# Optimization experiments

Measured on AMD Instinct MI355X. Metric: run time of the kernel, lower is better.

## Reference

```python
import jax, jax.numpy as jnp
import numpy as np

NEG_INF = -jnp.inf


def setup_inputs() -> dict:
    key = jax.random.key(0)
    ks = jax.random.split(key, 8)
    B, Lq, Lk, D, H = 8, 2048, 2048, 256, 128
    queries = jax.random.normal(ks[0], (B, Lq, D), dtype=jnp.float32)
    keys = jax.random.normal(ks[1], (B, Lk, D), dtype=jnp.float32)
    values_1 = jax.random.normal(ks[2], (B, Lk, D), dtype=jnp.float32)
    values_2 = jax.random.normal(ks[3], (B, Lq, D), dtype=jnp.float32)
    values_1_mask = jax.random.randint(ks[4], (B, Lk), 0, 2).astype(bool)
    values_2_mask = jax.random.randint(ks[5], (B, Lq), 0, 2).astype(bool)
    # xavier_normal for Linear(D -> H): std = sqrt(2/(D+H))
    std = float(np.sqrt(2.0 / (D + H)))
    Wq = jax.random.normal(ks[6], (H, D), dtype=jnp.float32) * std
    Wk = jax.random.normal(ks[7], (H, D), dtype=jnp.float32) * std
    scaling = jnp.ones((1, H), dtype=jnp.float32)
    return {
        "queries": queries, "keys": keys,
        "values_1": values_1, "values_1_mask": values_1_mask,
        "values_2": values_2, "values_2_mask": values_2_mask,
        "Wq": Wq, "Wk": Wk, "scaling": scaling,
    }


def reference(queries, keys, values_1, values_1_mask, values_2, values_2_mask, Wq, Wk, scaling):
    # projections + relu (eval mode: dropout inactive)
    pq = jax.nn.relu(jnp.einsum("bqd,hd->bqh", queries, Wq))        # [B,Lq,H]
    pk = jax.nn.relu(jnp.einsum("bkd,hd->bkh", keys, Wk)) * scaling  # [B,Lk,H]
    scores = jnp.einsum("bqh,bkh->bqk", pq, pk)                      # [B,Lq,Lk]

    # branch 2: softmax over queries axis of scores^T, masked by values_2_mask [B,Lq]
    scores_T = jnp.where(values_2_mask[:, None, :], NEG_INF, jnp.swapaxes(scores, 1, 2))  # [B,Lk,Lq]
    alpha_2 = jax.nn.softmax(scores_T, axis=2)
    output_2 = jnp.einsum("bkq,bqd->bkd", alpha_2, values_2)         # [B,Lk,D]

    # branch 1: softmax over keys axis, masked by values_1_mask [B,Lk]
    scores_1 = jnp.where(values_1_mask[:, None, :], NEG_INF, scores)  # [B,Lq,Lk]
    alpha_1 = jax.nn.softmax(scores_1, axis=2)
    output = jnp.einsum("bqk,bkd->bqd", alpha_1, values_1)           # [B,Lq,D]

    return (output, output_2)
```

## Files before the change

kernel.cpp:

```cpp
#include <hip/hip_runtime.h>
#include <cstdint>
#include <math.h>

#define B 8
#define L 2048
#define D 256
#define H 128

typedef __attribute__((ext_vector_type(8))) _Float16 half8;
typedef __attribute__((ext_vector_type(4))) _Float16 half4t;
typedef __attribute__((ext_vector_type(2))) _Float16 half2v;
typedef __attribute__((ext_vector_type(4))) float f32x4;
typedef unsigned short ushort;
typedef unsigned int uint;


__global__ void prep_kernel(const void* __restrict__ raw0,
                            const void* __restrict__ raw1,
                            const float* __restrict__ Wq,
                            const float* __restrict__ Wk,
                            float* __restrict__ fb1,
                            float* __restrict__ fb2,
                            _Float16* __restrict__ Wf) {
    const int t = threadIdx.x;
    const int z = blockIdx.y;
    {
        const void* raw = z ? raw1 : raw0;
        float* outb = z ? fb2 : fb1;
        const uint* wd = (const uint*)raw;
        __shared__ int flag;
        if (t == 0) flag = 0;
        __syncthreads();
        if (wd[t] > 1u) flag = 1;
        __syncthreads();
        const int base = blockIdx.x * 1024;
        if (flag) {
            const uint8_t* by = (const uint8_t*)raw;
#pragma unroll
            for (int j = 0; j < 4; ++j) {
                int i = base + t + 256 * j;
                outb[i] = by[i] ? -INFINITY : 0.f;
            }
        } else {
#pragma unroll
            for (int j = 0; j < 4; ++j) {
                int i = base + t + 256 * j;
                outb[i] = wd[i] ? -INFINITY : 0.f;
            }
        }
    }
    {
        const float* Wsrc = z ? Wk : Wq;
        const int chunk = blockIdx.x * 256 + t;
        const int h = chunk >> 5;
        const int d0 = (chunk & 31) * 8;
        float4 v0 = *(const float4*)(Wsrc + (size_t)h * 256 + d0);
        float4 v1 = *(const float4*)(Wsrc + (size_t)h * 256 + d0 + 4);
        half8 hv;
        hv[0] = (_Float16)v0.x; hv[1] = (_Float16)v0.y;
        hv[2] = (_Float16)v0.z; hv[3] = (_Float16)v0.w;
        hv[4] = (_Float16)v1.x; hv[5] = (_Float16)v1.y;
        hv[6] = (_Float16)v1.z; hv[7] = (_Float16)v1.w;
        const int db = d0 >> 5, dq = (d0 >> 3) & 3;
        size_t off = (size_t)z * 32768 +
                     ((size_t)((h >> 4) * 8 + db)) * 512 + dq * 128 + (h & 15) * 8;
        *(half8*)(Wf + off) = hv;
    }
}

__launch_bounds__(256, 2)
__global__ void proj_mfma_kernel(const float* __restrict__ queries,
                                 const float* __restrict__ keys,
                                 const _Float16* __restrict__ Wf,
                                 const float* __restrict__ scaling,
                                 _Float16* __restrict__ pqo,
                                 _Float16* __restrict__ pko) {
    const int t = threadIdx.x;
    const int w = t >> 6;
    const int lane = t & 63;
    const int l15 = lane & 15;
    const int quad = lane >> 4;
    const int z = blockIdx.z;
    const int half = blockIdx.y;
    const int r0 = blockIdx.x * 64;
    const float* in = z ? keys : queries;
    _Float16* outp = z ? pko : pqo;

    __shared__ __attribute__((aligned(16))) _Float16 Wl[32 * 512];
    __shared__ __attribute__((aligned(16))) _Float16 Af[4][8 * 512];

    {
        const _Float16* wsrc = Wf + ((size_t)z * 64 + half * 32) * 512;
#pragma unroll
        for (int i = 0; i < 8; ++i) {
            const int f = w * 8 + i;
            __builtin_amdgcn_global_load_lds(
                (const __attribute__((address_space(1))) uint*)(wsrc + f * 512 + lane * 8),
                (__attribute__((address_space(3))) uint*)(Wl + f * 512 + lane * 8),
                16, 0, 0);
        }
    }
    {
#pragma unroll
        for (int j = 0; j < 16; ++j) {
            const int idx = t + 256 * j;
            const int row = idx >> 6;
            const int c4 = idx & 63;
            float4 v = *(const float4*)(in + ((size_t)(r0 + row)) * 256 + c4 * 4);
            half4t h4;
            h4[0] = (_Float16)v.x; h4[1] = (_Float16)v.y;
            h4[2] = (_Float16)v.z; h4[3] = (_Float16)v.w;
            const int rt = row >> 4, rl = row & 15;
            const int d0 = c4 * 4;
            const int db = d0 >> 5, dq = (d0 >> 3) & 3, e = d0 & 7;
            *(half4t*)(&Af[rt][db * 512 + dq * 128 + rl * 8 + e]) = h4;
        }
    }
    __syncthreads();

    half8 a[8];
#pragma unroll
    for (int db = 0; db < 8; ++db)
        a[db] = *(const half8*)(&Af[w][db * 512 + lane * 8]);

    f32x4 acc[4];
#pragma unroll
    for (int hti = 0; hti < 4; ++hti) acc[hti] = (f32x4){0.f, 0.f, 0.f, 0.f};
#pragma unroll
    for (int db = 0; db < 8; ++db)
#pragma unroll
        for (int hti = 0; hti < 4; ++hti) {
            half8 bfrag = *(const half8*)(Wl + (hti * 8 + db) * 512 + lane * 8);
            acc[hti] = __builtin_amdgcn_mfma_f32_16x16x32_f16(a[db], bfrag, acc[hti], 0, 0, 0);
        }

    _Float16* S = Af[w];
#pragma unroll
    for (int hti = 0; hti < 4; ++hti) {
        const int hl_ = hti * 16 + l15;
        const int hb = hl_ >> 5, hq = (hl_ >> 3) & 3, e = hl_ & 7;
        const float scl = z ? scaling[half * 64 + hl_] : 1.f;
#pragma unroll
        for (int r = 0; r < 4; ++r) {
            float v = fmaxf(acc[hti][r], 0.f) * scl;
            S[hb * 512 + hq * 128 + (quad * 4 + r) * 8 + e] = (_Float16)v;
        }
    }
    const size_t grow16 = (size_t)(r0 >> 4) + w;
    _Float16* gout = outp + (grow16 * 4 + half * 2) * 512;
#pragma unroll
    for (int hb = 0; hb < 2; ++hb) {
        half8 vv = *(const half8*)(S + hb * 512 + lane * 8);
        *(half8*)(gout + hb * 512 + lane * 8) = vv;
    }
}

__global__ void vtrans_kernel(const float* __restrict__ v1,
                              const float* __restrict__ v2,
                              _Float16* __restrict__ vt1,
                              _Float16* __restrict__ vt2) {
    const int t = threadIdx.x;
    const int zz = blockIdx.z;
    const int b = zz & 7;
    const int which = zz >> 3;
    const float* src = (which ? v2 : v1) + (size_t)b * L * D;
    _Float16* dst = which ? vt2 : vt1;
    const int k0 = blockIdx.x * 64;
    const int d0 = blockIdx.y * 64;
    __shared__ float lt[64][65];
#pragma unroll
    for (int p = 0; p < 4; ++p) {
        int kr = p * 16 + (t >> 4);
        float4 v = *(const float4*)(src + (size_t)(k0 + kr) * D + d0 + (t & 15) * 4);
        lt[(t & 15) * 4 + 0][kr] = v.x;
        lt[(t & 15) * 4 + 1][kr] = v.y;
        lt[(t & 15) * 4 + 2][kr] = v.z;
        lt[(t & 15) * 4 + 3][kr] = v.w;
    }
    __syncthreads();
    const int d = t & 63;
    const int kk = (t >> 6) & 1;
    const int qp = t >> 7;
    const size_t tile = ((size_t)b * L + k0) / 32 + kk;
    const int ct = (d0 + d) >> 4;
    _Float16* base = dst + (tile * 16 + ct) * 512 + (d & 15) * 8;
#pragma unroll
    for (int s = 0; s < 2; ++s) {
        const int qv = qp * 2 + s;
        const float* lr = &lt[d][kk * 32 + qv * 8];
        half8 hv;
#pragma unroll
        for (int e = 0; e < 8; ++e) hv[e] = (_Float16)lr[e];
        *(half8*)(base + qv * 128) = hv;
    }
}

__launch_bounds__(256, 2)
__global__ void attn_fused_kernel(const _Float16* __restrict__ pqw,
                                  const _Float16* __restrict__ pkw,
                                  const float* __restrict__ fb1,
                                  const float* __restrict__ fb2,
                                  const _Float16* __restrict__ vt1,
                                  const _Float16* __restrict__ vt2,
                                  float* __restrict__ out) {
    const int t = threadIdx.x;
    const int w = t >> 6;
    const int lane = t & 63;
    const int l15 = lane & 15;
    const int quad = lane >> 4;
    const int bb = blockIdx.y;
    const int z = blockIdx.z;
    const int r0 = blockIdx.x * 64;
    const size_t bL = (size_t)bb * L;

    const _Float16* Qp = z ? pkw : pqw;
    const _Float16* Kp = z ? pqw : pkw;
    const _Float16* Vp = z ? vt2 : vt1;
    const float* fbb = (z ? fb2 : fb1) + bL;
    float* O = out + (z ? (size_t)B * L * D : 0);

    __shared__ __attribute__((aligned(16))) _Float16 klds[2][4096];
    __shared__ __attribute__((aligned(16))) _Float16 vlds[2][8192];
    __shared__ __attribute__((aligned(16))) _Float16 plds[4][512];

    auto stage = [&](int it, int buf) {
        const _Float16* ksrc = Kp + ((bL + it * 32) >> 4) * 2048;
#pragma unroll
        for (int i = 0; i < 2; ++i) {
            const int c = w * 2 + i;
            __builtin_amdgcn_global_load_lds(
                (const __attribute__((address_space(1))) uint*)(ksrc + c * 512 + lane * 8),
                (__attribute__((address_space(3))) uint*)(&klds[buf][c * 512] + lane * 8),
                16, 0, 0);
        }
        const _Float16* vsrc = Vp + ((bL + it * 32) >> 5) * (size_t)8192;
#pragma unroll
        for (int i = 0; i < 4; ++i) {
            const int c = w * 4 + i;
            __builtin_amdgcn_global_load_lds(
                (const __attribute__((address_space(1))) uint*)(vsrc + c * 512 + lane * 8),
                (__attribute__((address_space(3))) uint*)(&vlds[buf][c * 512] + lane * 8),
                16, 0, 0);
        }
    };

    half8 aq[4];
    {
        const _Float16* qb = Qp + ((bL + r0 + w * 16) >> 4) * 2048 + lane * 8;
#pragma unroll
        for (int hb = 0; hb < 4; ++hb) aq[hb] = *(const half8*)(qb + hb * 512);
    }

    stage(0, 0);
    float4 bc0 = *(const float4*)(fbb + quad * 4);
    float4 bc1 = *(const float4*)(fbb + 16 + quad * 4);
    stage(1, 1);

    asm volatile("s_waitcnt vmcnt(6)" ::: "memory");
    __builtin_amdgcn_sched_barrier(0);
    __builtin_amdgcn_s_barrier();
    __builtin_amdgcn_sched_barrier(0);

    f32x4 acc[16];
#pragma unroll
    for (int ct = 0; ct < 16; ++ct) acc[ct] = (f32x4){0.f, 0.f, 0.f, 0.f};
    float lsum = 0.f;
    float m = -1e30f;

    const int NT = 64;
#pragma unroll 2
    for (int it = 0; it < NT; ++it) {
        const int buf = it & 1;

        float4 bn0 = bc0, bn1 = bc1;
        if (it + 1 < NT) {
            bn0 = *(const float4*)(fbb + (it + 1) * 32 + quad * 4);
            bn1 = *(const float4*)(fbb + (it + 1) * 32 + 16 + quad * 4);
        }

        f32x4 s0 = (f32x4){0.f, 0.f, 0.f, 0.f};
        f32x4 s1 = (f32x4){0.f, 0.f, 0.f, 0.f};
#pragma unroll
        for (int hb = 0; hb < 4; ++hb) {
            half8 kf0 = *(const half8*)(&klds[buf][hb * 512 + lane * 8]);
            half8 kf1 = *(const half8*)(&klds[buf][2048 + hb * 512 + lane * 8]);
            s0 = __builtin_amdgcn_mfma_f32_16x16x32_f16(kf0, aq[hb], s0, 0, 0, 0);
            s1 = __builtin_amdgcn_mfma_f32_16x16x32_f16(kf1, aq[hb], s1, 0, 0, 0);
        }
        float sv0[4], sv1[4];
        float mt_ = -INFINITY;
#pragma unroll
        for (int r = 0; r < 4; ++r) {
            sv0[r] = s0[r] + ((const float*)&bc0)[r];
            sv1[r] = s1[r] + ((const float*)&bc1)[r];
            mt_ = fmaxf(mt_, fmaxf(sv0[r], sv1[r]));
        }
        mt_ = fmaxf(mt_, __shfl_xor(mt_, 16));
        mt_ = fmaxf(mt_, __shfl_xor(mt_, 32));

        if (!__all(mt_ <= m + 8.f)) {
            float mn = fmaxf(m, mt_);
            float sc = __expf(m - mn);
            m = mn;
            lsum *= sc;
#pragma unroll
            for (int ct = 0; ct < 16; ++ct) acc[ct] *= sc;
        }

        float psum = 0.f;
        float p0[4], p1[4];
#pragma unroll
        for (int r = 0; r < 4; ++r) {
            p0[r] = __expf(sv0[r] - m);
            p1[r] = __expf(sv1[r] - m);
            psum += p0[r] + p1[r];
        }
        lsum += psum;
        half2v q00; q00[0] = (_Float16)p0[0]; q00[1] = (_Float16)p0[1];
        half2v q01; q01[0] = (_Float16)p0[2]; q01[1] = (_Float16)p0[3];
        half2v q10; q10[0] = (_Float16)p1[0]; q10[1] = (_Float16)p1[1];
        half2v q11; q11[0] = (_Float16)p1[2]; q11[1] = (_Float16)p1[3];
        _Float16* pw = &plds[w][0];
        const int eb0 = (quad >> 1) * 128 + l15 * 8 + (quad & 1) * 4;
        const int eb1 = (2 + (quad >> 1)) * 128 + l15 * 8 + (quad & 1) * 4;
        *(half2v*)(pw + eb0) = q00;
        *(half2v*)(pw + eb0 + 2) = q01;
        *(half2v*)(pw + eb1) = q10;
        *(half2v*)(pw + eb1 + 2) = q11;
        half8 pfrag = *(const half8*)(pw + lane * 8);

#pragma unroll
        for (int ct = 0; ct < 16; ++ct) {
            half8 vf = *(const half8*)(&vlds[buf][ct * 512 + lane * 8]);
            acc[ct] = __builtin_amdgcn_mfma_f32_16x16x32_f16(vf, pfrag, acc[ct], 0, 0, 0);
        }

        bc0 = bn0; bc1 = bn1;

        if (it < NT - 1) {
            __builtin_amdgcn_s_barrier();
            __builtin_amdgcn_sched_barrier(0);
            if (it + 2 < NT) {
                stage(it + 2, buf);
                asm volatile("s_waitcnt vmcnt(6)" ::: "memory");
            } else {
                asm volatile("s_waitcnt vmcnt(0)" ::: "memory");
            }
            __builtin_amdgcn_sched_barrier(0);
            __builtin_amdgcn_s_barrier();
            __builtin_amdgcn_sched_barrier(0);
        }
    }

    lsum += __shfl_xor(lsum, 16);
    lsum += __shfl_xor(lsum, 32);
    const float inv = (lsum > 0.f) ? (1.f / lsum) : 0.f;

    const int qrow = r0 + w * 16 + l15;
    float* orow = O + (bL + qrow) * (size_t)D + quad * 4;
#pragma unroll
    for (int ct = 0; ct < 16; ++ct) {
        f32x4 v = acc[ct] * inv;
        *(f32x4*)(orow + ct * 16) = v;
    }
}

extern "C" void kernel_launch(void* const* d_in, const int* in_sizes, int n_in,
                              void* d_out, int out_size, void* d_ws, size_t ws_size,
                              hipStream_t stream) {
    const float* queries  = (const float*)d_in[0];
    const float* keys     = (const float*)d_in[1];
    const float* values_1 = (const float*)d_in[2];
    const void*  v1_mask  = d_in[3];
    const float* values_2 = (const float*)d_in[4];
    const void*  v2_mask  = d_in[5];
    const float* Wq       = (const float*)d_in[6];
    const float* Wk       = (const float*)d_in[7];
    const float* scaling  = (const float*)d_in[8];
    float* out = (float*)d_out;

    _Float16* pqw = (_Float16*)d_ws;
    _Float16* pkw = pqw + (size_t)B * L * H;
    _Float16* vt1 = pkw + (size_t)B * L * H;
    _Float16* vt2 = vt1 + (size_t)B * L * D;
    float* fb1   = (float*)(vt2 + (size_t)B * L * D);
    float* fb2   = fb1 + B * L;
    _Float16* Wf = (_Float16*)(fb2 + B * L);

    prep_kernel<<<dim3(16, 2), 256, 0, stream>>>(
        v1_mask, v2_mask, Wq, Wk, fb1, fb2, Wf);
    proj_mfma_kernel<<<dim3(B * L / 64, 2, 2), 256, 0, stream>>>(
        queries, keys, Wf, scaling, pqw, pkw);
    vtrans_kernel<<<dim3(L / 64, D / 64, B * 2), 256, 0, stream>>>(
        values_1, values_2, vt1, vt2);
    attn_fused_kernel<<<dim3(L / 64, B, 2), 256, 0, stream>>>(
        pqw, pkw, fb1, fb2, vt1, vt2, out);
}
```

Measured before the change: 227.4 us.

## Merge prep, projection and value-transpose kernels into one heterogeneous launch

Replaces three preprocessing kernels with a single kernel whose blocks are dispatched by block index to projection, value transpose or mask conversion work, interleaving projection and transpose blocks. Each projection block now converts its slice of the weights to fp16 itself instead of reading a pre-swizzled weight buffer, which removes the dependency on a separate prep launch. This cuts launch count and inter-kernel serialization, but projection blocks redo the weight conversion redundantly and all blocks share the larger LDS union footprint.

```diff
diff --git a/kernel.cpp b/kernel.cpp
--- a/kernel.cpp
+++ b/kernel.cpp
@@ -14,98 +14,66 @@
 typedef unsigned short ushort;
 typedef unsigned int uint;
 
-
-__global__ void prep_kernel(const void* __restrict__ raw0,
-                            const void* __restrict__ raw1,
-                            const float* __restrict__ Wq,
-                            const float* __restrict__ Wk,
-                            float* __restrict__ fb1,
-                            float* __restrict__ fb2,
-                            _Float16* __restrict__ Wf) {
+__launch_bounds__(256, 2)
+__global__ void pre_kernel(const float* __restrict__ queries,
+                           const float* __restrict__ keys,
+                           const float* __restrict__ Wq,
+                           const float* __restrict__ Wk,
+                           const float* __restrict__ scaling,
+                           const void* __restrict__ raw0,
+                           const void* __restrict__ raw1,
+                           const float* __restrict__ v1,
+                           const float* __restrict__ v2,
+                           _Float16* __restrict__ pqo,
+                           _Float16* __restrict__ pko,
+                           _Float16* __restrict__ vt1,
+                           _Float16* __restrict__ vt2,
+                           float* __restrict__ fb1,
+                           float* __restrict__ fb2) {
+    __shared__ __attribute__((aligned(16))) union {
+        struct { _Float16 Wl[32 * 512]; _Float16 Af[4][8 * 512]; } proj;
+        float lt[64][65];
+    } sh;
+    __shared__ int flag;
+
+    const int bid = blockIdx.x;
     const int t = threadIdx.x;
-    const int z = blockIdx.y;
-    {
-        const void* raw = z ? raw1 : raw0;
-        float* outb = z ? fb2 : fb1;
-        const uint* wd = (const uint*)raw;
-        __shared__ int flag;
-        if (t == 0) flag = 0;
-        __syncthreads();
-        if (wd[t] > 1u) flag = 1;
-        __syncthreads();
-        const int base = blockIdx.x * 1024;
-        if (flag) {
-            const uint8_t* by = (const uint8_t*)raw;
-#pragma unroll
-            for (int j = 0; j < 4; ++j) {
-                int i = base + t + 256 * j;
-                outb[i] = by[i] ? -INFINITY : 0.f;
-            }
-        } else {
-#pragma unroll
-            for (int j = 0; j < 4; ++j) {
-                int i = base + t + 256 * j;
-                outb[i] = wd[i] ? -INFINITY : 0.f;
-            }
-        }
-    }
-    {
+
+    if (bid < 3072 && (bid % 3) == 0) {
+        const int idx = bid / 3;
+        const int w = t >> 6;
+        const int lane = t & 63;
+        const int l15 = lane & 15;
+        const int quad = lane >> 4;
+        const int z = idx >> 9;
+        const int half = (idx >> 8) & 1;
+        const int r0 = (idx & 255) * 64;
+        const float* in = z ? keys : queries;
         const float* Wsrc = z ? Wk : Wq;
-        const int chunk = blockIdx.x * 256 + t;
-        const int h = chunk >> 5;
-        const int d0 = (chunk & 31) * 8;
-        float4 v0 = *(const float4*)(Wsrc + (size_t)h * 256 + d0);
-        float4 v1 = *(const float4*)(Wsrc + (size_t)h * 256 + d0 + 4);
-        half8 hv;
-        hv[0] = (_Float16)v0.x; hv[1] = (_Float16)v0.y;
-        hv[2] = (_Float16)v0.z; hv[3] = (_Float16)v0.w;
-        hv[4] = (_Float16)v1.x; hv[5] = (_Float16)v1.y;
-        hv[6] = (_Float16)v1.z; hv[7] = (_Float16)v1.w;
-        const int db = d0 >> 5, dq = (d0 >> 3) & 3;
-        size_t off = (size_t)z * 32768 +
-                     ((size_t)((h >> 4) * 8 + db)) * 512 + dq * 128 + (h & 15) * 8;
-        *(half8*)(Wf + off) = hv;
-    }
-}
-
-__launch_bounds__(256, 2)
-__global__ void proj_mfma_kernel(const float* __restrict__ queries,
-                                 const float* __restrict__ keys,
-                                 const _Float16* __restrict__ Wf,
-                                 const float* __restrict__ scaling,
-                                 _Float16* __restrict__ pqo,
-                                 _Float16* __restrict__ pko) {
-    const int t = threadIdx.x;
-    const int w = t >> 6;
-    const int lane = t & 63;
-    const int l15 = lane & 15;
-    const int quad = lane >> 4;
-    const int z = blockIdx.z;
-    const int half = blockIdx.y;
-    const int r0 = blockIdx.x * 64;
-    const float* in = z ? keys : queries;
-    _Float16* outp = z ? pko : pqo;
-
-    __shared__ __attribute__((aligned(16))) _Float16 Wl[32 * 512];
-    __shared__ __attribute__((aligned(16))) _Float16 Af[4][8 * 512];
-
-    {
-        const _Float16* wsrc = Wf + ((size_t)z * 64 + half * 32) * 512;
+        _Float16* outp = z ? pko : pqo;
+        _Float16* Wl = sh.proj.Wl;
+
 #pragma unroll
         for (int i = 0; i < 8; ++i) {
-            const int f = w * 8 + i;
-            __builtin_amdgcn_global_load_lds(
-                (const __attribute__((address_space(1))) uint*)(wsrc + f * 512 + lane * 8),
-                (__attribute__((address_space(3))) uint*)(Wl + f * 512 + lane * 8),
-                16, 0, 0);
-        }
-    }
-    {
+            const int cl = t + 256 * i;
+            const int hl = cl >> 5;
+            const int d0 = (cl & 31) * 8;
+            const float* wp = Wsrc + (size_t)(half * 64 + hl) * 256 + d0;
+            float4 v0 = *(const float4*)wp;
+            float4 v1w = *(const float4*)(wp + 4);
+            half8 hv;
+            hv[0] = (_Float16)v0.x; hv[1] = (_Float16)v0.y;
+            hv[2] = (_Float16)v0.z; hv[3] = (_Float16)v0.w;
+            hv[4] = (_Float16)v1w.x; hv[5] = (_Float16)v1w.y;
+            hv[6] = (_Float16)v1w.z; hv[7] = (_Float16)v1w.w;
+            const int db = d0 >> 5, dq = (d0 >> 3) & 3;
+            *(half8*)(Wl + ((hl >> 4) * 8 + db) * 512 + dq * 128 + (hl & 15) * 8) = hv;
+        }
 #pragma unroll
         for (int j = 0; j < 16; ++j) {
-            const int idx = t + 256 * j;
-            const int row = idx >> 6;
-            const int c4 = idx & 63;
+            const int idx2 = t + 256 * j;
+            const int row = idx2 >> 6;
+            const int c4 = idx2 & 63;
             float4 v = *(const float4*)(in + ((size_t)(r0 + row)) * 256 + c4 * 4);
             half4t h4;
             h4[0] = (_Float16)v.x; h4[1] = (_Float16)v.y;
@@ -113,85 +81,107 @@
             const int rt = row >> 4, rl = row & 15;
             const int d0 = c4 * 4;
             const int db = d0 >> 5, dq = (d0 >> 3) & 3, e = d0 & 7;
-            *(half4t*)(&Af[rt][db * 512 + dq * 128 + rl * 8 + e]) = h4;
-        }
-    }
-    __syncthreads();
-
-    half8 a[8];
-#pragma unroll
-    for (int db = 0; db < 8; ++db)
-        a[db] = *(const half8*)(&Af[w][db * 512 + lane * 8]);
-
-    f32x4 acc[4];
-#pragma unroll
-    for (int hti = 0; hti < 4; ++hti) acc[hti] = (f32x4){0.f, 0.f, 0.f, 0.f};
-#pragma unroll
-    for (int db = 0; db < 8; ++db)
+            *(half4t*)(&sh.proj.Af[rt][db * 512 + dq * 128 + rl * 8 + e]) = h4;
+        }
+        __syncthreads();
+
+        half8 a[8];
+#pragma unroll
+        for (int db = 0; db < 8; ++db)
+            a[db] = *(const half8*)(&sh.proj.Af[w][db * 512 + lane * 8]);
+
+        f32x4 acc[4];
+#pragma unroll
+        for (int hti = 0; hti < 4; ++hti) acc[hti] = (f32x4){0.f, 0.f, 0.f, 0.f};
+#pragma unroll
+        for (int db = 0; db < 8; ++db)
+#pragma unroll
+            for (int hti = 0; hti < 4; ++hti) {
+                half8 bfrag = *(const half8*)(Wl + (hti * 8 + db) * 512 + lane * 8);
+                acc[hti] = __builtin_amdgcn_mfma_f32_16x16x32_f16(a[db], bfrag, acc[hti], 0, 0, 0);
+            }
+
+        _Float16* S = sh.proj.Af[w];
 #pragma unroll
         for (int hti = 0; hti < 4; ++hti) {
-            half8 bfrag = *(const half8*)(Wl + (hti * 8 + db) * 512 + lane * 8);
-            acc[hti] = __builtin_amdgcn_mfma_f32_16x16x32_f16(a[db], bfrag, acc[hti], 0, 0, 0);
-        }
-
-    _Float16* S = Af[w];
-#pragma unroll
-    for (int hti = 0; hti < 4; ++hti) {
-        const int hl_ = hti * 16 + l15;
-        const int hb = hl_ >> 5, hq = (hl_ >> 3) & 3, e = hl_ & 7;
-        const float scl = z ? scaling[half * 64 + hl_] : 1.f;
-#pragma unroll
-        for (int r = 0; r < 4; ++r) {
-            float v = fmaxf(acc[hti][r], 0.f) * scl;
-            S[hb * 512 + hq * 128 + (quad * 4 + r) * 8 + e] = (_Float16)v;
-        }
-    }
-    const size_t grow16 = (size_t)(r0 >> 4) + w;
-    _Float16* gout = outp + (grow16 * 4 + half * 2) * 512;
-#pragma unroll
-    for (int hb = 0; hb < 2; ++hb) {
-        half8 vv = *(const half8*)(S + hb * 512 + lane * 8);
-        *(half8*)(gout + hb * 512 + lane * 8) = vv;
-    }
-}
-
-__global__ void vtrans_kernel(const float* __restrict__ v1,
-                              const float* __restrict__ v2,
-                              _Float16* __restrict__ vt1,
-                              _Float16* __restrict__ vt2) {
-    const int t = threadIdx.x;
-    const int zz = blockIdx.z;
-    const int b = zz & 7;
-    const int which = zz >> 3;
-    const float* src = (which ? v2 : v1) + (size_t)b * L * D;
-    _Float16* dst = which ? vt2 : vt1;
-    const int k0 = blockIdx.x * 64;
-    const int d0 = blockIdx.y * 64;
-    __shared__ float lt[64][65];
-#pragma unroll
-    for (int p = 0; p < 4; ++p) {
-        int kr = p * 16 + (t >> 4);
-        float4 v = *(const float4*)(src + (size_t)(k0 + kr) * D + d0 + (t & 15) * 4);
-        lt[(t & 15) * 4 + 0][kr] = v.x;
-        lt[(t & 15) * 4 + 1][kr] = v.y;
-        lt[(t & 15) * 4 + 2][kr] = v.z;
-        lt[(t & 15) * 4 + 3][kr] = v.w;
-    }
-    __syncthreads();
-    const int d = t & 63;
-    const int kk = (t >> 6) & 1;
-    const int qp = t >> 7;
-    const size_t tile = ((size_t)b * L + k0) / 32 + kk;
-    const int ct = (d0 + d) >> 4;
-    _Float16* base = dst + (tile * 16 + ct) * 512 + (d & 15) * 8;
-#pragma unroll
-    for (int s = 0; s < 2; ++s) {
-        const int qv = qp * 2 + s;
-        const float* lr = &lt[d][kk * 32 + qv * 8];
-        half8 hv;
-#pragma unroll
-        for (int e = 0; e < 8; ++e) hv[e] = (_Float16)lr[e];
-        *(half8*)(base + qv * 128) = hv;
+            const int hl_ = hti * 16 + l15;
+            const int hb = hl_ >> 5, hq = (hl_ >> 3) & 3, e = hl_ & 7;
+            const float scl = z ? scaling[half * 64 + hl_] : 1.f;
+#pragma unroll
+            for (int r = 0; r < 4; ++r) {
+                float v = fmaxf(acc[hti][r], 0.f) * scl;
+                S[hb * 512 + hq * 128 + (quad * 4 + r) * 8 + e] = (_Float16)v;
+            }
+        }
+        const size_t grow16 = (size_t)(r0 >> 4) + w;
+        _Float16* gout = outp + (grow16 * 4 + half * 2) * 512;
+#pragma unroll
+        for (int hb = 0; hb < 2; ++hb) {
+            half8 vv = *(const half8*)(S + hb * 512 + lane * 8);
+            *(half8*)(gout + hb * 512 + lane * 8) = vv;
+        }
+    } else if (bid < 3072) {
+        const int idx = (bid / 3) * 2 + (bid % 3) - 1;
+        const int zz = idx >> 7;
+        const int b = zz & 7;
+        const int which = zz >> 3;
+        const int x = idx & 31;
+        const int y = (idx >> 5) & 3;
+        const float* src = (which ? v2 : v1) + (size_t)b * L * D;
+        _Float16* dst = which ? vt2 : vt1;
+        const int k0 = x * 64;
+        const int d0 = y * 64;
+#pragma unroll
+        for (int p = 0; p < 4; ++p) {
+            int kr = p * 16 + (t >> 4);
+            float4 v = *(const float4*)(src + (size_t)(k0 + kr) * D + d0 + (t & 15) * 4);
+            sh.lt[(t & 15) * 4 + 0][kr] = v.x;
+            sh.lt[(t & 15) * 4 + 1][kr] = v.y;
+            sh.lt[(t & 15) * 4 + 2][kr] = v.z;
+            sh.lt[(t & 15) * 4 + 3][kr] = v.w;
+        }
+        __syncthreads();
+        const int d = t & 63;
+        const int kk = (t >> 6) & 1;
+        const int qp = t >> 7;
+        const size_t tile = ((size_t)b * L + k0) / 32 + kk;
+        const int ct = (d0 + d) >> 4;
+        _Float16* base = dst + (tile * 16 + ct) * 512 + (d & 15) * 8;
+#pragma unroll
+        for (int s = 0; s < 2; ++s) {
+            const int qv = qp * 2 + s;
+            const float* lr = &sh.lt[d][kk * 32 + qv * 8];
+            half8 hv;
+#pragma unroll
+            for (int e = 0; e < 8; ++e) hv[e] = (_Float16)lr[e];
+            *(half8*)(base + qv * 128) = hv;
+        }
+    } else {
+        const int idx = bid - 3072;
+        const int x = idx & 15;
+        const int z = idx >> 4;
+        const void* raw = z ? raw1 : raw0;
+        float* outb = z ? fb2 : fb1;
+        const uint* wd = (const uint*)raw;
+        if (t == 0) flag = 0;
+        __syncthreads();
+        if (wd[t] > 1u) flag = 1;
+        __syncthreads();
+        const int base = x * 1024;
+        if (flag) {
+            const uint8_t* by = (const uint8_t*)raw;
+#pragma unroll
+            for (int j = 0; j < 4; ++j) {
+                int i = base + t + 256 * j;
+                outb[i] = by[i] ? -INFINITY : 0.f;
+            }
+        } else {
+#pragma unroll
+            for (int j = 0; j < 4; ++j) {
+                int i = base + t + 256 * j;
+                outb[i] = wd[i] ? -INFINITY : 0.f;
+            }
+        }
     }
 }
 
@@ -385,14 +375,10 @@
     _Float16* vt2 = vt1 + (size_t)B * L * D;
     float* fb1   = (float*)(vt2 + (size_t)B * L * D);
     float* fb2   = fb1 + B * L;
-    _Float16* Wf = (_Float16*)(fb2 + B * L);
-
-    prep_kernel<<<dim3(16, 2), 256, 0, stream>>>(
-        v1_mask, v2_mask, Wq, Wk, fb1, fb2, Wf);
-    proj_mfma_kernel<<<dim3(B * L / 64, 2, 2), 256, 0, stream>>>(
-        queries, keys, Wf, scaling, pqw, pkw);
-    vtrans_kernel<<<dim3(L / 64, D / 64, B * 2), 256, 0, stream>>>(
-        values_1, values_2, vt1, vt2);
+
+    pre_kernel<<<3104, 256, 0, stream>>>(
+        queries, keys, Wq, Wk, scaling, v1_mask, v2_mask,
+        values_1, values_2, pqw, pkw, vt1, vt2, fb1, fb2);
     attn_fused_kernel<<<dim3(L / 64, B, 2), 256, 0, stream>>>(
         pqw, pkw, fb1, fb2, vt1, vt2, out);
 }
```

Measured after the change: 223.2 us. About the same (-1.8%).
